# Kernel tuning notes

Hardware: AMD Instinct MI355X
Metric: run time of the kernel (lower is better)

Reference implementation:

```python
import jax, jax.numpy as jnp
import numpy as np

EPS = 1e-5


def setup_inputs() -> dict:
    key = jax.random.key(0)
    S, B, I, H, D = 256, 512, 64, 128, 32
    ks = jax.random.split(key, 12)

    def w(k, shape, fan):
        return jax.random.normal(k, shape, jnp.float32) * (fan ** -0.5)

    lengths = jax.random.randint(ks[0], (B,), 1, S + 1)
    lengths = lengths.at[0].set(S)  # ensure max length == S
    return {
        'x': jax.random.normal(ks[1], (S, B, I), jnp.float32),
        'x_d': jax.random.normal(ks[2], (S, B, D), jnp.float32),
        'lengths': lengths,
        'bn_g': jnp.ones((I,), jnp.float32), 'bn_b': jnp.zeros((I,), jnp.float32),
        'bnd_g': jnp.ones((D,), jnp.float32), 'bnd_b': jnp.zeros((D,), jnp.float32),
        'Wih': w(ks[3], (3 * H, I), I), 'Whh': w(ks[4], (3 * H, H), H),
        'bih': jnp.zeros((3 * H,), jnp.float32), 'bhh': jnp.zeros((3 * H,), jnp.float32),
        'attn_W': w(ks[5], (H, H), H), 'attn_b': jnp.zeros((H,), jnp.float32),
        'W1': w(ks[6], (H, H + D), H + D), 'b1': jnp.zeros((H,), jnp.float32),
        'W2': w(ks[7], (H, H), H), 'b2': jnp.zeros((H,), jnp.float32),
        'W3': w(ks[8], (H, H), H), 'b3': jnp.zeros((H,), jnp.float32),
    }


def reference(x, x_d, lengths, bn_g, bn_b, bnd_g, bnd_b, Wih, Whh, bih, bhh,
              attn_W, attn_b, W1, b1, W2, b2, W3, b3):
    S, B, I = x.shape
    H = Whh.shape[1]
    mask = jnp.arange(S)[:, None] < lengths[None, :]          # [S,B] valid-token mask
    mf = mask[..., None].astype(x.dtype)                       # [S,B,1]
    cnt = mf.sum()

    def bn(v, g, b):  # training-mode BatchNorm1d over the packed (valid) tokens
        mu = (v * mf).sum((0, 1)) / cnt
        var = (((v - mu) * mf) ** 2).sum((0, 1)) / cnt
        return (v - mu) * jax.lax.rsqrt(var + EPS) * g + b

    xn = bn(x, bn_g, bn_b)
    xdn = bn(x_d, bnd_g, bnd_b)

    # --- GRU (PyTorch gate order r,z,n) over padded sequence with mask ---
    h0 = jnp.zeros((B, H), x.dtype)

    def step(h, inp):
        xt, mt = inp                                           # xt [B,I], mt [B,1]
        gi = xt @ Wih.T + bih
        gh = h @ Whh.T + bhh
        ir, iz, inn = jnp.split(gi, 3, axis=-1)
        hr, hz, hn = jnp.split(gh, 3, axis=-1)
        r = jax.nn.sigmoid(ir + hr)
        z = jax.nn.sigmoid(iz + hz)
        n = jnp.tanh(inn + r * hn)
        hnew = (1 - z) * n + z * h
        hnext = jnp.where(mt, hnew, h)                         # carry last valid state
        return hnext, jnp.where(mt, hnew, 0.0)                 # padded outputs are 0

    h_last, ys = jax.lax.scan(step, h0, (xn, mf))              # ys [S,B,H]

    # --- Dynamic_Attention: per step i only position j=i survives the causal
    # mask in column k=i, so the dim-0 softmax is over one element -> weight 1.
    # Keep fc in the graph (zero grad, same as torch) via a size-1 softmax. ---
    s = (ys @ attn_W.T + attn_b).sum(-1)                       # [S,B]
    attn = jax.nn.softmax(s[..., None, None], axis=-2)[..., 0, :]  # ones [S,B,1]
    y = attn * ys

    # --- per-token MLP (dropout = identity at eval), vectorized over all tokens ---
    z0 = jnp.concatenate([y, xdn], axis=-1)                    # [S,B,H+D]
    d = jax.nn.relu(z0 @ W1.T + b1)
    d = jax.nn.relu(d @ W2.T + b2)
    d = jax.nn.relu(d @ W3.T + b3)
    out = d * mf                                               # zero padded positions
    return out, h_last[None]                                   # hidden: [1,B,H]
```

## Files before the change

kernel.cpp:

```cpp
#include <hip/hip_runtime.h>
#include <hip/hip_bf16.h>

#define SS 256
#define BB 512
#define II 64
#define HH 128
#define DD 32

typedef __attribute__((ext_vector_type(8))) short short8;
typedef __attribute__((ext_vector_type(4))) float f32x4;

__device__ __forceinline__ short f2bf(float f) {
    unsigned u = __builtin_bit_cast(unsigned, f);
    u += 0x7FFFu + ((u >> 16) & 1u);
    return (short)(u >> 16);
}
__device__ __forceinline__ int pack2bf(float a, float b) {
    return (int)((((unsigned)(unsigned short)f2bf(b)) << 16) |
                  ((unsigned)(unsigned short)f2bf(a)));
}
__device__ __forceinline__ short8 load8bf(const float* p) {
    short8 r;
#pragma unroll
    for (int j = 0; j < 8; ++j) r[j] = f2bf(p[j]);
    return r;
}

__device__ __forceinline__ void sync_lds() {
    __builtin_amdgcn_s_waitcnt(0xc07f);
    __builtin_amdgcn_s_barrier();
}

__global__ __launch_bounds__(256) void stats_kernel(
    const float* __restrict__ x, const float* __restrict__ xd,
    const int* __restrict__ lengths, double* __restrict__ acc)
{
    __shared__ float red_s[256];
    __shared__ float red_q[256];
    const int rows = SS * BB;
    int blk = blockIdx.x;
    const float* v;
    int C, rpb, base;
    if (blk < 256) { v = x;  C = II; rpb = rows / 256; base = 0; }
    else           { v = xd; C = DD; rpb = rows / 128; base = 128; blk -= 256; }

    const int tid = threadIdx.x;
    const int c   = tid & (C - 1);
    const int rg  = tid / C;
    const int rpg = 256 / C;
    const int r0  = blk * rpb;
    const int r1  = r0 + rpb;
    float s = 0.f, q = 0.f;
    for (int r = r0 + rg; r < r1; r += rpg) {
        const int b  = r & (BB - 1);
        const int si = r >> 9;
        if (si < lengths[b]) {
            const float xv = v[(size_t)r * C + c];
            s += xv;
            q  = fmaf(xv, xv, q);
        }
    }
    red_s[tid] = s; red_q[tid] = q;
    __syncthreads();
    if (rg == 0) {
        for (int g = 1; g < rpg; ++g) { s += red_s[c + g * C]; q += red_q[c + g * C]; }
        atomicAdd(&acc[base + c],     (double)s);
        atomicAdd(&acc[base + C + c], (double)q);
    }
}

__global__ __launch_bounds__(128) void finalize_kernel(
    const int* __restrict__ lengths, const double* __restrict__ acc,
    const float* __restrict__ bn_g, const float* __restrict__ bn_b,
    const float* __restrict__ bnd_g, const float* __restrict__ bnd_b,
    float* __restrict__ der)
{
    __shared__ int redc[128];
    __shared__ double s_inv;
    const int tid = threadIdx.x;
    int cs = 0;
    for (int i = tid; i < BB; i += 128) cs += lengths[i];
    redc[tid] = cs;
    __syncthreads();
    if (tid == 0) {
        int tot = 0;
        for (int i = 0; i < 128; ++i) tot += redc[i];
        s_inv = 1.0 / (double)tot;
    }
    __syncthreads();
    const double inv = s_inv;
    if (tid < 64) {
        const double mu  = acc[tid] * inv;
        const double var = acc[64 + tid] * inv - mu * mu;
        const float  rs  = rsqrtf((float)(var + 1e-5));
        const float  a   = rs * bn_g[tid];
        der[tid]      = a;
        der[64 + tid] = bn_b[tid] - (float)mu * a;
    } else if (tid < 96) {
        const int i = tid - 64;
        const double mu  = acc[128 + i] * inv;
        const double var = acc[160 + i] * inv - mu * mu;
        const float  rs  = rsqrtf((float)(var + 1e-5));
        const float  a   = rs * bnd_g[i];
        der[128 + i] = a;
        der[160 + i] = bnd_b[i] - (float)mu * a;
    }
}

__global__ __launch_bounds__(512, 2) void gru_kernel(
    const float* __restrict__ x, const int* __restrict__ lengths,
    const float* __restrict__ Wih, const float* __restrict__ Whh,
    const float* __restrict__ bih, const float* __restrict__ bhh,
    const float* __restrict__ der,
    float* __restrict__ ys, float* __restrict__ hlast)
{
    __shared__ __align__(16) short hbf[2][16 * 136];
    __shared__ __align__(16) short xbf[2][16 * 72];

    const int tid  = threadIdx.x;
    const int w    = tid >> 6;
    const int l    = tid & 63;
    const int col  = l & 15;
    const int quad = l >> 4;
    const int b0   = blockIdx.x * 16;
    const int ur   = 16 * w + col;
    const int g0   = 16 * w + quad * 4;

    short8 WR[6], WZ[6], WNh[4], WNx[2];
#pragma unroll
    for (int ks = 0; ks < 4; ++ks) {
        const int ko = ks * 32 + quad * 8;
        WR[ks]  = load8bf(&Whh[(size_t)ur * HH + ko]);
        WZ[ks]  = load8bf(&Whh[(size_t)(HH + ur) * HH + ko]);
        WNh[ks] = load8bf(&Whh[(size_t)(2 * HH + ur) * HH + ko]);
    }
#pragma unroll
    for (int ks = 0; ks < 2; ++ks) {
        const int ko = ks * 32 + quad * 8;
        WR[4 + ks] = load8bf(&Wih[(size_t)ur * II + ko]);
        WZ[4 + ks] = load8bf(&Wih[(size_t)(HH + ur) * II + ko]);
        WNx[ks]    = load8bf(&Wih[(size_t)(2 * HH + ur) * II + ko]);
    }
    float br_[4], bz_[4], bnh_[4], bnx_[4];
#pragma unroll
    for (int r = 0; r < 4; ++r) {
        const int g = g0 + r;
        br_[r]  = bih[g] + bhh[g];
        bz_[r]  = bih[HH + g] + bhh[HH + g];
        bnh_[r] = bhh[2 * HH + g];
        bnx_[r] = bih[2 * HH + g];
    }
    const int len = lengths[b0 + col];

    const int srow = tid >> 5, scol = (tid & 31) * 2;
    const float ax0 = der[scol],      ax1 = der[scol + 1];
    const float cx0 = der[64 + scol], cx1 = der[64 + scol + 1];

    for (int i = tid; i < 16 * 136 / 2; i += 512) ((int*)hbf[0])[i] = 0;
    float hreg[4] = {0.f, 0.f, 0.f, 0.f};
    {
        const float2 xv = *(const float2*)&x[(size_t)(b0 + srow) * II + scol];
        *(int*)&xbf[0][srow * 72 + scol] =
            pack2bf(fmaf(xv.x, ax0, cx0), fmaf(xv.y, ax1, cx1));
    }
    sync_lds();

    int p = 0;
    for (int t = 0; t < SS; ++t) {
        float2 xv;
        if (t + 1 < SS)
            xv = *(const float2*)&x[(size_t)((t + 1) * BB + b0 + srow) * II + scol];

        short8 Hf[4];
#pragma unroll
        for (int ks = 0; ks < 4; ++ks)
            Hf[ks] = *(const short8*)&hbf[p][col * 136 + ks * 32 + quad * 8];
        const short8 XN0 = *(const short8*)&xbf[p][col * 72 + quad * 8];
        const short8 XN1 = *(const short8*)&xbf[p][col * 72 + 32 + quad * 8];

        f32x4 ar  = {br_[0],  br_[1],  br_[2],  br_[3]};
        f32x4 az  = {bz_[0],  bz_[1],  bz_[2],  bz_[3]};
        f32x4 anh = {bnh_[0], bnh_[1], bnh_[2], bnh_[3]};
        f32x4 anx = {bnx_[0], bnx_[1], bnx_[2], bnx_[3]};
#pragma unroll
        for (int ks = 0; ks < 4; ++ks) {
            ar  = __builtin_amdgcn_mfma_f32_16x16x32_bf16(WR[ks],  Hf[ks], ar,  0, 0, 0);
            az  = __builtin_amdgcn_mfma_f32_16x16x32_bf16(WZ[ks],  Hf[ks], az,  0, 0, 0);
            anh = __builtin_amdgcn_mfma_f32_16x16x32_bf16(WNh[ks], Hf[ks], anh, 0, 0, 0);
        }
        ar  = __builtin_amdgcn_mfma_f32_16x16x32_bf16(WR[4],  XN0, ar,  0, 0, 0);
        ar  = __builtin_amdgcn_mfma_f32_16x16x32_bf16(WR[5],  XN1, ar,  0, 0, 0);
        az  = __builtin_amdgcn_mfma_f32_16x16x32_bf16(WZ[4],  XN0, az,  0, 0, 0);
        az  = __builtin_amdgcn_mfma_f32_16x16x32_bf16(WZ[5],  XN1, az,  0, 0, 0);
        anx = __builtin_amdgcn_mfma_f32_16x16x32_bf16(WNx[0], XN0, anx, 0, 0, 0);
        anx = __builtin_amdgcn_mfma_f32_16x16x32_bf16(WNx[1], XN1, anx, 0, 0, 0);

        const bool valid = (t < len);
#pragma unroll
        for (int r = 0; r < 4; ++r) {
            const float rg = __builtin_amdgcn_rcpf(1.f + __expf(-ar[r]));
            const float zg = __builtin_amdgcn_rcpf(1.f + __expf(-az[r]));
            const float nv = anx[r] + rg * anh[r];
            const float ng = 1.f - 2.f * __builtin_amdgcn_rcpf(1.f + __expf(2.f * nv));
            const float hnew = (1.f - zg) * ng + zg * hreg[r];
            hreg[r] = valid ? hnew : hreg[r];
        }
        {
            float4 o;
            o.x = hreg[0]; o.y = hreg[1]; o.z = hreg[2]; o.w = hreg[3];
            *(float4*)&ys[((size_t)t * BB + b0 + col) * HH + g0] = o;
            int2 pk;
            pk.x = pack2bf(hreg[0], hreg[1]);
            pk.y = pack2bf(hreg[2], hreg[3]);
            *(int2*)&hbf[p ^ 1][col * 136 + g0] = pk;
        }
        if (t + 1 < SS)
            *(int*)&xbf[p ^ 1][srow * 72 + scol] =
                pack2bf(fmaf(xv.x, ax0, cx0), fmaf(xv.y, ax1, cx1));

        sync_lds();
        p ^= 1;
    }

    {
        float4 hl;
        hl.x = hreg[0]; hl.y = hreg[1]; hl.z = hreg[2]; hl.w = hreg[3];
        *(float4*)&hlast[(size_t)(b0 + col) * HH + g0] = hl;
    }
}

__global__ __launch_bounds__(512, 2) void mlp_kernel(
    const float* __restrict__ xd, const int* __restrict__ lengths,
    const float* __restrict__ W1, const float* __restrict__ b1v,
    const float* __restrict__ W2, const float* __restrict__ b2v,
    const float* __restrict__ W3, const float* __restrict__ b3v,
    const float* __restrict__ der, float* io)
{
    __shared__ __align__(16) short z0[2][16 * 168];
    __shared__ __align__(16) short d1b[2][16 * 136];
    __shared__ __align__(16) short d2b[2][16 * 136];

    const int tid  = threadIdx.x;
    const int w    = tid >> 6;
    const int l    = tid & 63;
    const int col  = l & 15;
    const int quad = l >> 4;
    const int ur   = 16 * w + col;
    const int g0   = 16 * w + quad * 4;

    short8 F1[5], F2[4], F3[4];
#pragma unroll
    for (int ks = 0; ks < 5; ++ks)
        F1[ks] = load8bf(&W1[(size_t)ur * 160 + ks * 32 + quad * 8]);
#pragma unroll
    for (int ks = 0; ks < 4; ++ks) {
        const int ko = ks * 32 + quad * 8;
        F2[ks] = load8bf(&W2[(size_t)ur * HH + ko]);
        F3[ks] = load8bf(&W3[(size_t)ur * HH + ko]);
    }
    float bb1_[4], bb2_[4], bb3_[4];
#pragma unroll
    for (int r = 0; r < 4; ++r) {
        bb1_[r] = b1v[g0 + r]; bb2_[r] = b2v[g0 + r]; bb3_[r] = b3v[g0 + r];
    }

    const int yrow = tid >> 5, yc = (tid & 31) * 4;
    const int drow = tid >> 4, dcol = (tid & 15) * 2;
    float ad0 = 0.f, ad1 = 0.f, cd0 = 0.f, cd1 = 0.f;
    if (tid < 256) {
        ad0 = der[128 + dcol]; ad1 = der[128 + dcol + 1];
        cd0 = der[160 + dcol]; cd1 = der[160 + dcol + 1];
    }

    const int tile0 = blockIdx.x * 16;

    {
        const size_t tok0 = (size_t)tile0 * 16;
        const float4 yv = *(const float4*)&io[(tok0 + yrow) * HH + yc];
        int2 pk;
        pk.x = pack2bf(yv.x, yv.y);
        pk.y = pack2bf(yv.z, yv.w);
        *(int2*)&z0[0][yrow * 168 + yc] = pk;
        if (tid < 256) {
            const float2 dv = *(const float2*)&xd[(tok0 + drow) * DD + dcol];
            *(int*)&z0[0][drow * 168 + HH + dcol] =
                pack2bf(fmaf(dv.x, ad0, cd0), fmaf(dv.y, ad1, cd1));
        }
    }
    sync_lds();

    int p = 0;
    for (int it = 0; it <= 17; ++it) {
        float4 yv; float2 dv;
        const int nt = it + 1;
        if (nt <= 15) {
            const size_t tok0n = (size_t)(tile0 + nt) * 16;
            yv = *(const float4*)&io[(tok0n + yrow) * HH + yc];
            if (tid < 256) dv = *(const float2*)&xd[(tok0n + drow) * DD + dcol];
        }

        f32x4 a1 = {bb1_[0], bb1_[1], bb1_[2], bb1_[3]};
#pragma unroll
        for (int ks = 0; ks < 5; ++ks)
            a1 = __builtin_amdgcn_mfma_f32_16x16x32_bf16(
                F1[ks], *(const short8*)&z0[p][col * 168 + ks * 32 + quad * 8], a1, 0, 0, 0);
        {
            int2 pk;
            pk.x = pack2bf(fmaxf(a1[0], 0.f), fmaxf(a1[1], 0.f));
            pk.y = pack2bf(fmaxf(a1[2], 0.f), fmaxf(a1[3], 0.f));
            *(int2*)&d1b[p ^ 1][col * 136 + g0] = pk;
        }

        f32x4 a2 = {bb2_[0], bb2_[1], bb2_[2], bb2_[3]};
#pragma unroll
        for (int ks = 0; ks < 4; ++ks)
            a2 = __builtin_amdgcn_mfma_f32_16x16x32_bf16(
                F2[ks], *(const short8*)&d1b[p][col * 136 + ks * 32 + quad * 8], a2, 0, 0, 0);
        {
            int2 pk;
            pk.x = pack2bf(fmaxf(a2[0], 0.f), fmaxf(a2[1], 0.f));
            pk.y = pack2bf(fmaxf(a2[2], 0.f), fmaxf(a2[3], 0.f));
            *(int2*)&d2b[p ^ 1][col * 136 + g0] = pk;
        }

        f32x4 a3 = {bb3_[0], bb3_[1], bb3_[2], bb3_[3]};
#pragma unroll
        for (int ks = 0; ks < 4; ++ks)
            a3 = __builtin_amdgcn_mfma_f32_16x16x32_bf16(
                F3[ks], *(const short8*)&d2b[p][col * 136 + ks * 32 + quad * 8], a3, 0, 0, 0);
        if (it >= 2) {
            const int tok0 = (tile0 + it - 2) * 16;
            const int tI = tok0 >> 9;
            const int bI = tok0 & (BB - 1);
            const bool v = tI < lengths[bI + col];
            float4 o;
            o.x = v ? fmaxf(a3[0], 0.f) : 0.f;
            o.y = v ? fmaxf(a3[1], 0.f) : 0.f;
            o.z = v ? fmaxf(a3[2], 0.f) : 0.f;
            o.w = v ? fmaxf(a3[3], 0.f) : 0.f;
            *(float4*)&io[((size_t)tok0 + col) * HH + g0] = o;
        }

        if (nt <= 15) {
            int2 pk;
            pk.x = pack2bf(yv.x, yv.y);
            pk.y = pack2bf(yv.z, yv.w);
            *(int2*)&z0[p ^ 1][yrow * 168 + yc] = pk;
            if (tid < 256)
                *(int*)&z0[p ^ 1][drow * 168 + HH + dcol] =
                    pack2bf(fmaf(dv.x, ad0, cd0), fmaf(dv.y, ad1, cd1));
        }
        sync_lds();
        p ^= 1;
    }
}

extern "C" void kernel_launch(void* const* d_in, const int* in_sizes, int n_in,
                              void* d_out, int out_size, void* d_ws, size_t ws_size,
                              hipStream_t stream)
{
    (void)in_sizes; (void)n_in; (void)out_size; (void)ws_size;
    const float* x     = (const float*)d_in[0];
    const float* xd    = (const float*)d_in[1];
    const int*   lens  = (const int*)d_in[2];
    const float* bn_g  = (const float*)d_in[3];
    const float* bn_b  = (const float*)d_in[4];
    const float* bnd_g = (const float*)d_in[5];
    const float* bnd_b = (const float*)d_in[6];
    const float* Wih   = (const float*)d_in[7];
    const float* Whh   = (const float*)d_in[8];
    const float* bih   = (const float*)d_in[9];
    const float* bhh   = (const float*)d_in[10];
    const float* W1    = (const float*)d_in[13];
    const float* b1    = (const float*)d_in[14];
    const float* W2    = (const float*)d_in[15];
    const float* b2    = (const float*)d_in[16];
    const float* W3    = (const float*)d_in[17];
    const float* b3    = (const float*)d_in[18];

    float* out   = (float*)d_out;
    float* hlast = out + (size_t)SS * BB * HH;

    double* acc = (double*)d_ws;
    float*  der = (float*)((char*)d_ws + 2048);

    hipMemsetAsync(d_ws, 0, 2048, stream);

    stats_kernel<<<384, 256, 0, stream>>>(x, xd, lens, acc);
    finalize_kernel<<<1, 128, 0, stream>>>(lens, acc, bn_g, bn_b, bnd_g, bnd_b, der);

    gru_kernel<<<BB / 16, 512, 0, stream>>>(x, lens, Wih, Whh, bih, bhh, der,
                                            out, hlast);

    mlp_kernel<<<512, 512, 0, stream>>>(xd, lens, W1, b1, W2, b2, W3, b3,
                                        der, out);
}
```

Baseline: 470.0 us.

## Give GRU blocks 32 batch rows, stage bf16 hidden states, shrink MLP tiles

The GRU kernel now handles 32 batch rows per block: two groups of four waves, each wave computing two 16-row gate tiles. This halves the block count from 32 to 16 and raises MFMA work per LDS sync. GRU outputs can go to a bf16 workspace buffer when it is large enough, which cuts the write and re-read traffic between the GRU and MLP kernels. The MLP kernel processes 8 tiles per block across 1024 blocks with a higher occupancy hint. The risk is that only 16 blocks run the serial recurrence, so far fewer CUs are used and each step carries more work.

Result: slower. 840.3 us (+78.8%).

```diff
diff --git a/kernel.cpp b/kernel.cpp
--- a/kernel.cpp
+++ b/kernel.cpp
@@ -112,129 +112,153 @@
     const float* __restrict__ Wih, const float* __restrict__ Whh,
     const float* __restrict__ bih, const float* __restrict__ bhh,
     const float* __restrict__ der,
-    float* __restrict__ ys, float* __restrict__ hlast)
+    short* __restrict__ ybf, float* __restrict__ yf32,
+    float* __restrict__ hlast, int use_ws)
 {
-    __shared__ __align__(16) short hbf[2][16 * 136];
-    __shared__ __align__(16) short xbf[2][16 * 72];
+    __shared__ __align__(16) short hbf[2][2][16 * 136];
+    __shared__ __align__(16) short xbf[2][2][16 * 72];
 
     const int tid  = threadIdx.x;
     const int w    = tid >> 6;
     const int l    = tid & 63;
     const int col  = l & 15;
     const int quad = l >> 4;
-    const int b0   = blockIdx.x * 16;
-    const int ur   = 16 * w + col;
-    const int g0   = 16 * w + quad * 4;
-
-    short8 WR[6], WZ[6], WNh[4], WNx[2];
-#pragma unroll
-    for (int ks = 0; ks < 4; ++ks) {
-        const int ko = ks * 32 + quad * 8;
-        WR[ks]  = load8bf(&Whh[(size_t)ur * HH + ko]);
-        WZ[ks]  = load8bf(&Whh[(size_t)(HH + ur) * HH + ko]);
-        WNh[ks] = load8bf(&Whh[(size_t)(2 * HH + ur) * HH + ko]);
-    }
-#pragma unroll
-    for (int ks = 0; ks < 2; ++ks) {
-        const int ko = ks * 32 + quad * 8;
-        WR[4 + ks] = load8bf(&Wih[(size_t)ur * II + ko]);
-        WZ[4 + ks] = load8bf(&Wih[(size_t)(HH + ur) * II + ko]);
-        WNx[ks]    = load8bf(&Wih[(size_t)(2 * HH + ur) * II + ko]);
-    }
-    float br_[4], bz_[4], bnh_[4], bnx_[4];
-#pragma unroll
-    for (int r = 0; r < 4; ++r) {
-        const int g = g0 + r;
-        br_[r]  = bih[g] + bhh[g];
-        bz_[r]  = bih[HH + g] + bhh[HH + g];
-        bnh_[r] = bhh[2 * HH + g];
-        bnx_[r] = bih[2 * HH + g];
-    }
-    const int len = lengths[b0 + col];
-
-    const int srow = tid >> 5, scol = (tid & 31) * 2;
-    const float ax0 = der[scol],      ax1 = der[scol + 1];
-    const float cx0 = der[64 + scol], cx1 = der[64 + scol + 1];
-
-    for (int i = tid; i < 16 * 136 / 2; i += 512) ((int*)hbf[0])[i] = 0;
-    float hreg[4] = {0.f, 0.f, 0.f, 0.f};
+    const int g    = w >> 2;
+    const int ws3  = w & 3;
+    const int b0   = blockIdx.x * 32;
+    const int tokb = b0 + 16 * g + col;
+
+    short8 WR[2][6], WZ[2][6], WNh[2][4], WNx[2][2];
+#pragma unroll
+    for (int mt = 0; mt < 2; ++mt) {
+        const int ur = 32 * ws3 + 16 * mt + col;
+#pragma unroll
+        for (int ks = 0; ks < 4; ++ks) {
+            const int ko = ks * 32 + quad * 8;
+            WR[mt][ks]  = load8bf(&Whh[(size_t)ur * HH + ko]);
+            WZ[mt][ks]  = load8bf(&Whh[(size_t)(HH + ur) * HH + ko]);
+            WNh[mt][ks] = load8bf(&Whh[(size_t)(2 * HH + ur) * HH + ko]);
+        }
+#pragma unroll
+        for (int ks = 0; ks < 2; ++ks) {
+            const int ko = ks * 32 + quad * 8;
+            WR[mt][4 + ks] = load8bf(&Wih[(size_t)ur * II + ko]);
+            WZ[mt][4 + ks] = load8bf(&Wih[(size_t)(HH + ur) * II + ko]);
+            WNx[mt][ks]    = load8bf(&Wih[(size_t)(2 * HH + ur) * II + ko]);
+        }
+    }
+    float br_[2][4], bz_[2][4], bnh_[2][4], bnx_[2][4];
+#pragma unroll
+    for (int mt = 0; mt < 2; ++mt)
+#pragma unroll
+        for (int r = 0; r < 4; ++r) {
+            const int gg = 32 * ws3 + 16 * mt + 4 * quad + r;
+            br_[mt][r]  = bih[gg] + bhh[gg];
+            bz_[mt][r]  = bih[HH + gg] + bhh[HH + gg];
+            bnh_[mt][r] = bhh[2 * HH + gg];
+            bnx_[mt][r] = bih[2 * HH + gg];
+        }
+    const int len = lengths[tokb];
+
+    const int srow = tid >> 4, scol = (tid & 15) * 4;
+    const float4 a4 = *(const float4*)&der[scol];
+    const float4 c4 = *(const float4*)&der[64 + scol];
+
+    for (int i = tid; i < 2 * 16 * 136 / 2; i += 512) ((int*)hbf[0])[i] = 0;
+    float hreg[2][4] = {{0.f,0.f,0.f,0.f},{0.f,0.f,0.f,0.f}};
     {
-        const float2 xv = *(const float2*)&x[(size_t)(b0 + srow) * II + scol];
-        *(int*)&xbf[0][srow * 72 + scol] =
-            pack2bf(fmaf(xv.x, ax0, cx0), fmaf(xv.y, ax1, cx1));
+        const float4 xv = *(const float4*)&x[(size_t)(b0 + srow) * II + scol];
+        int2 pk;
+        pk.x = pack2bf(fmaf(xv.x, a4.x, c4.x), fmaf(xv.y, a4.y, c4.y));
+        pk.y = pack2bf(fmaf(xv.z, a4.z, c4.z), fmaf(xv.w, a4.w, c4.w));
+        *(int2*)&xbf[0][srow >> 4][(srow & 15) * 72 + scol] = pk;
     }
     sync_lds();
 
     int p = 0;
     for (int t = 0; t < SS; ++t) {
-        float2 xv;
+        float4 xv;
         if (t + 1 < SS)
-            xv = *(const float2*)&x[(size_t)((t + 1) * BB + b0 + srow) * II + scol];
+            xv = *(const float4*)&x[(size_t)((t + 1) * BB + b0 + srow) * II + scol];
 
         short8 Hf[4];
 #pragma unroll
         for (int ks = 0; ks < 4; ++ks)
-            Hf[ks] = *(const short8*)&hbf[p][col * 136 + ks * 32 + quad * 8];
-        const short8 XN0 = *(const short8*)&xbf[p][col * 72 + quad * 8];
-        const short8 XN1 = *(const short8*)&xbf[p][col * 72 + 32 + quad * 8];
-
-        f32x4 ar  = {br_[0],  br_[1],  br_[2],  br_[3]};
-        f32x4 az  = {bz_[0],  bz_[1],  bz_[2],  bz_[3]};
-        f32x4 anh = {bnh_[0], bnh_[1], bnh_[2], bnh_[3]};
-        f32x4 anx = {bnx_[0], bnx_[1], bnx_[2], bnx_[3]};
-#pragma unroll
-        for (int ks = 0; ks < 4; ++ks) {
-            ar  = __builtin_amdgcn_mfma_f32_16x16x32_bf16(WR[ks],  Hf[ks], ar,  0, 0, 0);
-            az  = __builtin_amdgcn_mfma_f32_16x16x32_bf16(WZ[ks],  Hf[ks], az,  0, 0, 0);
-            anh = __builtin_amdgcn_mfma_f32_16x16x32_bf16(WNh[ks], Hf[ks], anh, 0, 0, 0);
-        }
-        ar  = __builtin_amdgcn_mfma_f32_16x16x32_bf16(WR[4],  XN0, ar,  0, 0, 0);
-        ar  = __builtin_amdgcn_mfma_f32_16x16x32_bf16(WR[5],  XN1, ar,  0, 0, 0);
-        az  = __builtin_amdgcn_mfma_f32_16x16x32_bf16(WZ[4],  XN0, az,  0, 0, 0);
-        az  = __builtin_amdgcn_mfma_f32_16x16x32_bf16(WZ[5],  XN1, az,  0, 0, 0);
-        anx = __builtin_amdgcn_mfma_f32_16x16x32_bf16(WNx[0], XN0, anx, 0, 0, 0);
-        anx = __builtin_amdgcn_mfma_f32_16x16x32_bf16(WNx[1], XN1, anx, 0, 0, 0);
+            Hf[ks] = *(const short8*)&hbf[p][g][col * 136 + ks * 32 + quad * 8];
+        const short8 XN0 = *(const short8*)&xbf[p][g][col * 72 + quad * 8];
+        const short8 XN1 = *(const short8*)&xbf[p][g][col * 72 + 32 + quad * 8];
+
+        f32x4 ar[2], az[2], anh[2], anx[2];
+#pragma unroll
+        for (int mt = 0; mt < 2; ++mt) {
+            ar[mt]  = (f32x4){br_[mt][0],  br_[mt][1],  br_[mt][2],  br_[mt][3]};
+            az[mt]  = (f32x4){bz_[mt][0],  bz_[mt][1],  bz_[mt][2],  bz_[mt][3]};
+            anh[mt] = (f32x4){bnh_[mt][0], bnh_[mt][1], bnh_[mt][2], bnh_[mt][3]};
+            anx[mt] = (f32x4){bnx_[mt][0], bnx_[mt][1], bnx_[mt][2], bnx_[mt][3]};
+#pragma unroll
+            for (int ks = 0; ks < 4; ++ks) {
+                ar[mt]  = __builtin_amdgcn_mfma_f32_16x16x32_bf16(WR[mt][ks],  Hf[ks], ar[mt],  0, 0, 0);
+                az[mt]  = __builtin_amdgcn_mfma_f32_16x16x32_bf16(WZ[mt][ks],  Hf[ks], az[mt],  0, 0, 0);
+                anh[mt] = __builtin_amdgcn_mfma_f32_16x16x32_bf16(WNh[mt][ks], Hf[ks], anh[mt], 0, 0, 0);
+            }
+            ar[mt]  = __builtin_amdgcn_mfma_f32_16x16x32_bf16(WR[mt][4],  XN0, ar[mt],  0, 0, 0);
+            ar[mt]  = __builtin_amdgcn_mfma_f32_16x16x32_bf16(WR[mt][5],  XN1, ar[mt],  0, 0, 0);
+            az[mt]  = __builtin_amdgcn_mfma_f32_16x16x32_bf16(WZ[mt][4],  XN0, az[mt],  0, 0, 0);
+            az[mt]  = __builtin_amdgcn_mfma_f32_16x16x32_bf16(WZ[mt][5],  XN1, az[mt],  0, 0, 0);
+            anx[mt] = __builtin_amdgcn_mfma_f32_16x16x32_bf16(WNx[mt][0], XN0, anx[mt], 0, 0, 0);
+            anx[mt] = __builtin_amdgcn_mfma_f32_16x16x32_bf16(WNx[mt][1], XN1, anx[mt], 0, 0, 0);
+        }
 
         const bool valid = (t < len);
 #pragma unroll
-        for (int r = 0; r < 4; ++r) {
-            const float rg = __builtin_amdgcn_rcpf(1.f + __expf(-ar[r]));
-            const float zg = __builtin_amdgcn_rcpf(1.f + __expf(-az[r]));
-            const float nv = anx[r] + rg * anh[r];
-            const float ng = 1.f - 2.f * __builtin_amdgcn_rcpf(1.f + __expf(2.f * nv));
-            const float hnew = (1.f - zg) * ng + zg * hreg[r];
-            hreg[r] = valid ? hnew : hreg[r];
-        }
-        {
-            float4 o;
-            o.x = hreg[0]; o.y = hreg[1]; o.z = hreg[2]; o.w = hreg[3];
-            *(float4*)&ys[((size_t)t * BB + b0 + col) * HH + g0] = o;
+        for (int mt = 0; mt < 2; ++mt) {
+#pragma unroll
+            for (int r = 0; r < 4; ++r) {
+                const float rg = __builtin_amdgcn_rcpf(1.f + __expf(-ar[mt][r]));
+                const float zg = __builtin_amdgcn_rcpf(1.f + __expf(-az[mt][r]));
+                const float nv = anx[mt][r] + rg * anh[mt][r];
+                const float ng = 1.f - 2.f * __builtin_amdgcn_rcpf(1.f + __expf(2.f * nv));
+                const float hnew = (1.f - zg) * ng + zg * hreg[mt][r];
+                hreg[mt][r] = valid ? hnew : hreg[mt][r];
+            }
             int2 pk;
-            pk.x = pack2bf(hreg[0], hreg[1]);
-            pk.y = pack2bf(hreg[2], hreg[3]);
-            *(int2*)&hbf[p ^ 1][col * 136 + g0] = pk;
-        }
-        if (t + 1 < SS)
-            *(int*)&xbf[p ^ 1][srow * 72 + scol] =
-                pack2bf(fmaf(xv.x, ax0, cx0), fmaf(xv.y, ax1, cx1));
-
+            pk.x = pack2bf(hreg[mt][0], hreg[mt][1]);
+            pk.y = pack2bf(hreg[mt][2], hreg[mt][3]);
+            *(int2*)&hbf[p ^ 1][g][col * 136 + 32 * ws3 + 16 * mt + 4 * quad] = pk;
+            if (use_ws) {
+                *(int2*)&ybf[(((size_t)t * BB + tokb) << 7) + 32 * ws3 + 16 * mt + 4 * quad] = pk;
+            } else {
+                float4 o;
+                o.x = hreg[mt][0]; o.y = hreg[mt][1]; o.z = hreg[mt][2]; o.w = hreg[mt][3];
+                *(float4*)&yf32[(((size_t)t * BB + tokb) << 7) + 32 * ws3 + 16 * mt + 4 * quad] = o;
+            }
+        }
+        if (t + 1 < SS) {
+            int2 pk;
+            pk.x = pack2bf(fmaf(xv.x, a4.x, c4.x), fmaf(xv.y, a4.y, c4.y));
+            pk.y = pack2bf(fmaf(xv.z, a4.z, c4.z), fmaf(xv.w, a4.w, c4.w));
+            *(int2*)&xbf[p ^ 1][srow >> 4][(srow & 15) * 72 + scol] = pk;
+        }
         sync_lds();
         p ^= 1;
     }
 
-    {
+#pragma unroll
+    for (int mt = 0; mt < 2; ++mt) {
         float4 hl;
-        hl.x = hreg[0]; hl.y = hreg[1]; hl.z = hreg[2]; hl.w = hreg[3];
-        *(float4*)&hlast[(size_t)(b0 + col) * HH + g0] = hl;
-    }
-}
-
-__global__ __launch_bounds__(512, 2) void mlp_kernel(
+        hl.x = hreg[mt][0]; hl.y = hreg[mt][1];
+        hl.z = hreg[mt][2]; hl.w = hreg[mt][3];
+        *(float4*)&hlast[((size_t)tokb << 7) + 32 * ws3 + 16 * mt + 4 * quad] = hl;
+    }
+}
+
+__global__ __launch_bounds__(512, 4) void mlp_kernel(
     const float* __restrict__ xd, const int* __restrict__ lengths,
     const float* __restrict__ W1, const float* __restrict__ b1v,
     const float* __restrict__ W2, const float* __restrict__ b2v,
     const float* __restrict__ W3, const float* __restrict__ b3v,
-    const float* __restrict__ der, float* io)
+    const float* __restrict__ der, const short* __restrict__ ybf,
+    float* io, int use_ws)
 {
     __shared__ __align__(16) short z0[2][16 * 168];
     __shared__ __align__(16) short d1b[2][16 * 136];
@@ -272,15 +296,18 @@
         cd0 = der[160 + dcol]; cd1 = der[160 + dcol + 1];
     }
 
-    const int tile0 = blockIdx.x * 16;
+    const int tile0 = blockIdx.x * 8;
 
     {
         const size_t tok0 = (size_t)tile0 * 16;
-        const float4 yv = *(const float4*)&io[(tok0 + yrow) * HH + yc];
-        int2 pk;
-        pk.x = pack2bf(yv.x, yv.y);
-        pk.y = pack2bf(yv.z, yv.w);
-        *(int2*)&z0[0][yrow * 168 + yc] = pk;
+        if (use_ws) {
+            const int2 yv = *(const int2*)&ybf[((tok0 + yrow) << 7) + yc];
+            *(int2*)&z0[0][yrow * 168 + yc] = yv;
+        } else {
+            const float4 yv = *(const float4*)&io[((tok0 + yrow) << 7) + yc];
+            int2 pk; pk.x = pack2bf(yv.x, yv.y); pk.y = pack2bf(yv.z, yv.w);
+            *(int2*)&z0[0][yrow * 168 + yc] = pk;
+        }
         if (tid < 256) {
             const float2 dv = *(const float2*)&xd[(tok0 + drow) * DD + dcol];
             *(int*)&z0[0][drow * 168 + HH + dcol] =
@@ -290,12 +317,13 @@
     sync_lds();
 
     int p = 0;
-    for (int it = 0; it <= 17; ++it) {
-        float4 yv; float2 dv;
+    for (int it = 0; it <= 9; ++it) {
+        int2 yvi; float4 yvf; float2 dv;
         const int nt = it + 1;
-        if (nt <= 15) {
+        if (nt <= 7) {
             const size_t tok0n = (size_t)(tile0 + nt) * 16;
-            yv = *(const float4*)&io[(tok0n + yrow) * HH + yc];
+            if (use_ws) yvi = *(const int2*)&ybf[((tok0n + yrow) << 7) + yc];
+            else        yvf = *(const float4*)&io[((tok0n + yrow) << 7) + yc];
             if (tid < 256) dv = *(const float2*)&xd[(tok0n + drow) * DD + dcol];
         }
 
@@ -338,14 +366,16 @@
             o.y = v ? fmaxf(a3[1], 0.f) : 0.f;
             o.z = v ? fmaxf(a3[2], 0.f) : 0.f;
             o.w = v ? fmaxf(a3[3], 0.f) : 0.f;
-            *(float4*)&io[((size_t)tok0 + col) * HH + g0] = o;
-        }
-
-        if (nt <= 15) {
-            int2 pk;
-            pk.x = pack2bf(yv.x, yv.y);
-            pk.y = pack2bf(yv.z, yv.w);
-            *(int2*)&z0[p ^ 1][yrow * 168 + yc] = pk;
+            *(float4*)&io[(((size_t)tok0 + col) << 7) + g0] = o;
+        }
+
+        if (nt <= 7) {
+            if (use_ws) {
+                *(int2*)&z0[p ^ 1][yrow * 168 + yc] = yvi;
+            } else {
+                int2 pk; pk.x = pack2bf(yvf.x, yvf.y); pk.y = pack2bf(yvf.z, yvf.w);
+                *(int2*)&z0[p ^ 1][yrow * 168 + yc] = pk;
+            }
             if (tid < 256)
                 *(int*)&z0[p ^ 1][drow * 168 + HH + dcol] =
                     pack2bf(fmaf(dv.x, ad0, cd0), fmaf(dv.y, ad1, cd1));
@@ -359,7 +389,7 @@
                               void* d_out, int out_size, void* d_ws, size_t ws_size,
                               hipStream_t stream)
 {
-    (void)in_sizes; (void)n_in; (void)out_size; (void)ws_size;
+    (void)in_sizes; (void)n_in; (void)out_size;
     const float* x     = (const float*)d_in[0];
     const float* xd    = (const float*)d_in[1];
     const int*   lens  = (const int*)d_in[2];
@@ -383,15 +413,19 @@
 
     double* acc = (double*)d_ws;
     float*  der = (float*)((char*)d_ws + 2048);
+    short*  ybf = (short*)((char*)d_ws + 4096);
+
+    const size_t need = 4096 + (size_t)SS * BB * HH * sizeof(short);
+    const int use_ws = (ws_size >= need) ? 1 : 0;
 
     hipMemsetAsync(d_ws, 0, 2048, stream);
 
     stats_kernel<<<384, 256, 0, stream>>>(x, xd, lens, acc);
     finalize_kernel<<<1, 128, 0, stream>>>(lens, acc, bn_g, bn_b, bnd_g, bnd_b, der);
 
-    gru_kernel<<<BB / 16, 512, 0, stream>>>(x, lens, Wih, Whh, bih, bhh, der,
-                                            out, hlast);
-
-    mlp_kernel<<<512, 512, 0, stream>>>(xd, lens, W1, b1, W2, b2, W3, b3,
-                                        der, out);
-}
+    gru_kernel<<<BB / 32, 512, 0, stream>>>(x, lens, Wih, Whh, bih, bhh, der,
+                                            ybf, out, hlast, use_ws);
+
+    mlp_kernel<<<1024, 512, 0, stream>>>(xd, lens, W1, b1, W2, b2, W3, b3,
+                                         der, ybf, out, use_ws);
+}
```
